# Kernel optimization log

Hardware: AMD Instinct MI355X
Metric: run time of the kernel (lower is better)

## Reference

```python
import jax, jax.numpy as jnp
import numpy as np

N_CELL, N_IO, D, H = 100000, 2000, 128, 4
C = D // H  # head dim = 32
E_CC, E_CIO, E_IOC = 600000, 50000, 50000


def _gat(x_src, x_dst, ei, W, a_src, a_dst, b, n_dst):
    """PyG GATConv (shared lin, concat=True, add_self_loops=False, eval mode)."""
    s, d = ei[0], ei[1]
    hs = (x_src @ W).reshape(-1, H, C)   # [Ns,H,C]
    hd = (x_dst @ W).reshape(-1, H, C)   # [Nd,H,C]
    al_s = (hs * a_src).sum(-1)          # [Ns,H]
    al_d = (hd * a_dst).sum(-1)          # [Nd,H]
    e = jax.nn.leaky_relu(al_s[s] + al_d[d], 0.2)            # [E,H]
    m = jax.ops.segment_max(e, d, num_segments=n_dst)
    m = jnp.where(jnp.isfinite(m), m, 0.0)
    ex = jnp.exp(e - m[d])
    den = jax.ops.segment_sum(ex, d, num_segments=n_dst)
    alpha = ex / (den[d] + 1e-16)                            # segment softmax
    out = jax.ops.segment_sum(alpha[:, :, None] * hs[s], d, num_segments=n_dst)
    return out.reshape(n_dst, D) + b


def _transform(x, Wt, bt, g, be):
    h = x @ Wt + bt
    mu = h.mean(-1, keepdims=True)
    var = h.var(-1, keepdims=True)
    h = (h - mu) * jax.lax.rsqrt(var + 1e-5) * g + be
    return x + jax.nn.relu(h)


def setup_inputs() -> dict:
    key = jax.random.key(0)
    ks = jax.random.split(key, 32)
    sc = 1.0 / np.sqrt(D)
    inp = {
        'x_cell': jax.random.normal(ks[0], (N_CELL, D), jnp.float32),
        'x_io': jax.random.normal(ks[1], (N_IO, D), jnp.float32),
        'ei_cc': jnp.stack([jax.random.randint(ks[2], (E_CC,), 0, N_CELL),
                             jax.random.randint(ks[3], (E_CC,), 0, N_CELL)]).astype(jnp.int32),
        'ei_cio': jnp.stack([jax.random.randint(ks[4], (E_CIO,), 0, N_CELL),
                              jax.random.randint(ks[5], (E_CIO,), 0, N_IO)]).astype(jnp.int32),
        'ei_ioc': jnp.stack([jax.random.randint(ks[6], (E_IOC,), 0, N_IO),
                              jax.random.randint(ks[7], (E_IOC,), 0, N_CELL)]).astype(jnp.int32),
    }
    i = 8
    for rel in ('cc', 'cio', 'ioc'):
        inp[f'W_{rel}'] = jax.random.normal(ks[i], (D, D), jnp.float32) * sc; i += 1
        inp[f'as_{rel}'] = jax.random.normal(ks[i], (H, C), jnp.float32) * sc; i += 1
        inp[f'ad_{rel}'] = jax.random.normal(ks[i], (H, C), jnp.float32) * sc; i += 1
        inp[f'b_{rel}'] = jnp.zeros((D,), jnp.float32)
    for nt in ('cell', 'io'):
        inp[f'Wt_{nt}'] = jax.random.normal(ks[i], (D, D), jnp.float32) * sc; i += 1
        inp[f'bt_{nt}'] = jnp.zeros((D,), jnp.float32)
        inp[f'g_{nt}'] = jnp.ones((D,), jnp.float32)
        inp[f'be_{nt}'] = jnp.zeros((D,), jnp.float32)
    return inp


def reference(x_cell, x_io,
              W_cc, as_cc, ad_cc, b_cc,
              W_cio, as_cio, ad_cio, b_cio,
              W_ioc, as_ioc, ad_ioc, b_ioc,
              Wt_cell, bt_cell, g_cell, be_cell,
              Wt_io, bt_io, g_io, be_io,
              ei_cc, ei_cio, ei_ioc):
    # HeteroConv with aggr='sum': cell gets cc + io->cell; io gets cell->io
    out_cell = _gat(x_cell, x_cell, ei_cc, W_cc, as_cc, ad_cc, b_cc, N_CELL) \
             + _gat(x_io, x_cell, ei_ioc, W_ioc, as_ioc, ad_ioc, b_ioc, N_CELL)
    out_io = _gat(x_cell, x_io, ei_cio, W_cio, as_cio, ad_cio, b_cio, N_IO)
    out_cell = _transform(out_cell, Wt_cell, bt_cell, g_cell, be_cell)
    out_io = _transform(out_io, Wt_io, bt_io, g_io, be_io)
    return out_cell, out_io
```

## Files before the change

### kernel.cpp

```cpp
#include <hip/hip_runtime.h>


#define NC   100000
#define NIO  2000
#define ECC  600000
#define ECIO 50000
#define EIOC 50000

#define PAD_CC   100352
#define PAD_IO   2048
#define NTOT_PAD (2 * PAD_CC + PAD_IO)
#define SCAN_NBLK (NTOT_PAD / 2048)

typedef unsigned short u16;
typedef short bf16x8 __attribute__((ext_vector_type(8)));
typedef float f32x4 __attribute__((ext_vector_type(4)));

static __device__ __forceinline__ u16 f2bf(float x) {
  unsigned u = __float_as_uint(x);
  return (u16)((u + 0x7FFFu + ((u >> 16) & 1u)) >> 16);
}
static __device__ __forceinline__ float bf2f(u16 h) {
  return __uint_as_float(((unsigned)h) << 16);
}

__global__ __launch_bounds__(256) void prep_w(
    const float* __restrict__ W0, const float* __restrict__ W1,
    const float* __restrict__ W2, const float* __restrict__ W3,
    const float* __restrict__ W4, u16* __restrict__ wt,
    const float* __restrict__ ad_ioc, const float* __restrict__ ad_cio,
    float* __restrict__ Vd_ioc, float* __restrict__ Vd_cio) {
  int t = blockIdx.x * blockDim.x + threadIdx.x;
  int mat = t >> 14, e = t & 16383;
  int k = e >> 7, n = e & 127;
  const float* W = (mat == 0) ? W0 : (mat == 1) ? W1 : (mat == 2) ? W2
                 : (mat == 3) ? W3 : W4;
  float x = W[k * 128 + n];
  u16 h = f2bf(x);
  u16 l = f2bf(x - bf2f(h));
  int kt = k >> 6, kl = k & 63, kg = kl >> 3, j = kl & 7;
  int off = (kt * 128 + n) * 64 + ((kg ^ (n & 7)) * 8) + j;
  u16* base = wt + (size_t)mat * 32768;
  base[off] = h;
  base[16384 + off] = l;

  if (t < 1024) {
    const float* Wv = (t < 512) ? W2 : W1;
    const float* ad = (t < 512) ? ad_ioc : ad_cio;
    float*       V  = (t < 512) ? Vd_ioc : Vd_cio;
    int i = t & 511, kk = i >> 2, hh = i & 3;
    float s = 0.f;
#pragma unroll
    for (int c = 0; c < 32; ++c) s += Wv[kk * 128 + hh * 32 + c] * ad[hh * 32 + c];
    V[kk * 4 + hh] = s;
  }
}

template <int MODE>
__global__ __launch_bounds__(256) void mfma_gemm(
    const float* __restrict__ A, int M,
    const u16* __restrict__ WT,
    float* __restrict__ Out,
    const float* __restrict__ as_vec, float* __restrict__ als,
    const float* __restrict__ ad_vec, float* __restrict__ ald,
    const float* __restrict__ bt, const float* __restrict__ gv_,
    const float* __restrict__ bev) {
  __shared__ u16 smem[32768];
  u16* Ah = smem;
  u16* Al = smem + 8192;
  u16* Wh = smem + 16384;
  u16* Wl = smem + 24576;
  const int tid = threadIdx.x;
  const int bm = blockIdx.x * 128;
  const int lane = tid & 63;
  const int wv = tid >> 6;
  const int qm = wv >> 1, qn = wv & 1;
  const int l15 = lane & 15, l4 = lane >> 4;

  f32x4 acc[4][4];
#pragma unroll
  for (int mi = 0; mi < 4; ++mi)
#pragma unroll
    for (int ni = 0; ni < 4; ++ni) acc[mi][ni] = {0.f, 0.f, 0.f, 0.f};

  for (int kt = 0; kt < 2; ++kt) {
#pragma unroll
    for (int q = 0; q < 4; ++q) {
      int flat = q * 256 + tid;
      int row = flat >> 3, kg = flat & 7;
      int grow = bm + row;
      float f[8];
      if (grow < M) {
        float4 v0 = *(const float4*)(A + (size_t)grow * 128 + kt * 64 + kg * 8);
        float4 v1 = *(const float4*)(A + (size_t)grow * 128 + kt * 64 + kg * 8 + 4);
        f[0] = v0.x; f[1] = v0.y; f[2] = v0.z; f[3] = v0.w;
        f[4] = v1.x; f[5] = v1.y; f[6] = v1.z; f[7] = v1.w;
      } else {
#pragma unroll
        for (int j = 0; j < 8; ++j) f[j] = 0.f;
      }
      union { bf16x8 v; u16 u[8]; } ph, pl;
#pragma unroll
      for (int j = 0; j < 8; ++j) {
        u16 h = f2bf(f[j]);
        ph.u[j] = h;
        pl.u[j] = f2bf(f[j] - bf2f(h));
      }
      int off = row * 64 + ((kg ^ (row & 7)) * 8);
      *(bf16x8*)(Ah + off) = ph.v;
      *(bf16x8*)(Al + off) = pl.v;
    }
    {
      const int4* sh = (const int4*)(WT + kt * 8192);
      const int4* sl = (const int4*)(WT + 16384 + kt * 8192);
#pragma unroll
      for (int q = 0; q < 4; ++q) {
        int idx = q * 256 + tid;
        ((int4*)Wh)[idx] = sh[idx];
        ((int4*)Wl)[idx] = sl[idx];
      }
    }
    __syncthreads();
#pragma unroll
    for (int kk = 0; kk < 2; ++kk) {
      bf16x8 ah[4], al[4], bh[4], bl[4];
#pragma unroll
      for (int mi = 0; mi < 4; ++mi) {
        int row = qm * 64 + mi * 16 + l15;
        int off = row * 64 + (((kk * 4 + l4) ^ (row & 7)) * 8);
        ah[mi] = *(const bf16x8*)(Ah + off);
        al[mi] = *(const bf16x8*)(Al + off);
      }
#pragma unroll
      for (int ni = 0; ni < 4; ++ni) {
        int n = qn * 64 + ni * 16 + l15;
        int off = n * 64 + (((kk * 4 + l4) ^ (n & 7)) * 8);
        bh[ni] = *(const bf16x8*)(Wh + off);
        bl[ni] = *(const bf16x8*)(Wl + off);
      }
#pragma unroll
      for (int mi = 0; mi < 4; ++mi)
#pragma unroll
        for (int ni = 0; ni < 4; ++ni) {
          acc[mi][ni] = __builtin_amdgcn_mfma_f32_16x16x32_bf16(
              ah[mi], bh[ni], acc[mi][ni], 0, 0, 0);
          acc[mi][ni] = __builtin_amdgcn_mfma_f32_16x16x32_bf16(
              ah[mi], bl[ni], acc[mi][ni], 0, 0, 0);
          acc[mi][ni] = __builtin_amdgcn_mfma_f32_16x16x32_bf16(
              al[mi], bh[ni], acc[mi][ni], 0, 0, 0);
        }
    }
    __syncthreads();
  }

  if (MODE == 1) {
#pragma unroll
    for (int mi = 0; mi < 4; ++mi)
#pragma unroll
      for (int ni = 0; ni < 4; ++ni)
#pragma unroll
        for (int r = 0; r < 4; ++r) {
          int grow = bm + qm * 64 + mi * 16 + l4 * 4 + r;
          if (grow < M)
            Out[(size_t)grow * 128 + qn * 64 + ni * 16 + l15] = acc[mi][ni][r];
        }
    float asv[4], adv[4];
#pragma unroll
    for (int ni = 0; ni < 4; ++ni) {
      asv[ni] = as_vec[qn * 64 + ni * 16 + l15];
      adv[ni] = (ald != nullptr) ? ad_vec[qn * 64 + ni * 16 + l15] : 0.f;
    }
#pragma unroll
    for (int mi = 0; mi < 4; ++mi)
#pragma unroll
      for (int r = 0; r < 4; ++r) {
        float s0 = acc[mi][0][r] * asv[0] + acc[mi][1][r] * asv[1];
        float s1 = acc[mi][2][r] * asv[2] + acc[mi][3][r] * asv[3];
        float t0 = acc[mi][0][r] * adv[0] + acc[mi][1][r] * adv[1];
        float t1 = acc[mi][2][r] * adv[2] + acc[mi][3][r] * adv[3];
#pragma unroll
        for (int off = 1; off < 16; off <<= 1) {
          s0 += __shfl_xor(s0, off);
          s1 += __shfl_xor(s1, off);
          t0 += __shfl_xor(t0, off);
          t1 += __shfl_xor(t1, off);
        }
        if (l15 == 0) {
          int grow = bm + qm * 64 + mi * 16 + l4 * 4 + r;
          if (grow < M) {
            als[(size_t)grow * 4 + qn * 2]     = s0;
            als[(size_t)grow * 4 + qn * 2 + 1] = s1;
            if (ald != nullptr) {
              ald[(size_t)grow * 4 + qn * 2]     = t0;
              ald[(size_t)grow * 4 + qn * 2 + 1] = t1;
            }
          }
        }
      }
  } else {
    float btv[4], gvv[4], bevv[4];
#pragma unroll
    for (int ni = 0; ni < 4; ++ni) {
      int col = qn * 64 + ni * 16 + l15;
      btv[ni] = bt[col]; gvv[ni] = gv_[col]; bevv[ni] = bev[col];
    }
    float* part = (float*)(smem + 16384);
#pragma unroll
    for (int mi = 0; mi < 4; ++mi)
#pragma unroll
      for (int r = 0; r < 4; ++r) {
        float hs = 0.f, hss = 0.f;
#pragma unroll
        for (int ni = 0; ni < 4; ++ni) {
          float hv = acc[mi][ni][r] + btv[ni];
          hs += hv; hss += hv * hv;
        }
#pragma unroll
        for (int off = 1; off < 16; off <<= 1) {
          hs += __shfl_xor(hs, off);
          hss += __shfl_xor(hss, off);
        }
        if (l15 == 0) {
          int rl = qm * 64 + mi * 16 + l4 * 4 + r;
          part[rl * 4 + qn * 2]     = hs;
          part[rl * 4 + qn * 2 + 1] = hss;
        }
      }
    __syncthreads();
#pragma unroll
    for (int mi = 0; mi < 4; ++mi)
#pragma unroll
      for (int r = 0; r < 4; ++r) {
        int rl = qm * 64 + mi * 16 + l4 * 4 + r;
        int grow = bm + rl;
        float s  = part[rl * 4] + part[rl * 4 + 2];
        float ss = part[rl * 4 + 1] + part[rl * 4 + 3];
        float mu = s * (1.f / 128.f);
        float var = ss * (1.f / 128.f) - mu * mu;
        float rs = rsqrtf(var + 1e-5f);
        if (grow < M) {
#pragma unroll
          for (int ni = 0; ni < 4; ++ni) {
            int col = qn * 64 + ni * 16 + l15;
            float y = A[(size_t)grow * 128 + col];
            float hv = acc[mi][ni][r] + btv[ni];
            float hn = (hv - mu) * rs * gvv[ni] + bevv[ni];
            Out[(size_t)grow * 128 + col] = y + (hn > 0.f ? hn : 0.f);
          }
        }
      }
  }
}

__global__ __launch_bounds__(256) void gemv_all(
    const float* __restrict__ x_cell, const float* __restrict__ x_io,
    const float* __restrict__ Vd_ioc, const float* __restrict__ Vd_cio,
    float* __restrict__ ald_ioc, float* __restrict__ ald_cio) {
  int lane = threadIdx.x & 63;
  int wid  = (blockIdx.x * blockDim.x + threadIdx.x) >> 6;
  int nw   = (gridDim.x * blockDim.x) >> 6;
  for (int row = wid; row < NC + NIO; row += nw) {
    const float* xr; const float* Vd; float* o;
    if (row < NC) { xr = x_cell + (size_t)row * 128; Vd = Vd_ioc; o = ald_ioc + 4 * (size_t)row; }
    else { int r2 = row - NC; xr = x_io + (size_t)r2 * 128; Vd = Vd_cio; o = ald_cio + 4 * (size_t)r2; }
    float4 v0 = *(const float4*)(Vd + 8 * lane);
    float4 v1 = *(const float4*)(Vd + 8 * lane + 4);
    float2 xv = *(const float2*)(xr + 2 * lane);
    float p0 = xv.x * v0.x + xv.y * v1.x;
    float p1 = xv.x * v0.y + xv.y * v1.y;
    float p2 = xv.x * v0.z + xv.y * v1.z;
    float p3 = xv.x * v0.w + xv.y * v1.w;
#pragma unroll
    for (int off = 32; off >= 1; off >>= 1) {
      p0 += __shfl_xor(p0, off);
      p1 += __shfl_xor(p1, off);
      p2 += __shfl_xor(p2, off);
      p3 += __shfl_xor(p3, off);
    }
    if (lane == 0) *(float4*)o = make_float4(p0, p1, p2, p3);
  }
}

__global__ void hist_all(const int* __restrict__ ei_cc, const int* __restrict__ ei_ioc,
                         const int* __restrict__ ei_cio,
                         int* __restrict__ c_cc, int* __restrict__ c_ioc,
                         int* __restrict__ c_cio) {
  int i = blockIdx.x * blockDim.x + threadIdx.x;
  if (i < ECC) atomicAdd(c_cc + ei_cc[ECC + i], 1);
  else if (i < ECC + EIOC) { int j = i - ECC; atomicAdd(c_ioc + ei_ioc[EIOC + j], 1); }
  else if (i < ECC + EIOC + ECIO) { int j = i - ECC - EIOC; atomicAdd(c_cio + ei_cio[ECIO + j], 1); }
}

__global__ __launch_bounds__(1024) void scan_p1(const int* __restrict__ cnt,
                                                int* __restrict__ bsum) {
  int b = blockIdx.x, t = threadIdx.x;
  int2 c = *(const int2*)(cnt + (size_t)b * 2048 + 2 * t);
  int v = c.x + c.y;
#pragma unroll
  for (int off = 1; off < 64; off <<= 1) v += __shfl_xor(v, off);
  __shared__ int ws_[16];
  if ((t & 63) == 0) ws_[t >> 6] = v;
  __syncthreads();
  if (t < 16) {
    int x = ws_[t];
#pragma unroll
    for (int off = 1; off < 16; off <<= 1) x += __shfl_xor(x, off);
    if (t == 0) bsum[b] = x;
  }
}

__global__ __launch_bounds__(1024) void scan_p3(
    const int* __restrict__ cnt, const int* __restrict__ bsum,
    int* __restrict__ roff_cc, int* __restrict__ wp_cc,
    int* __restrict__ roff_ioc, int* __restrict__ wp_ioc,
    int* __restrict__ roff_cio, int* __restrict__ wp_cio) {
  int b = blockIdx.x, t = threadIdx.x;
  __shared__ int topbase_s;
  if (t < 64) {
    int s = 0;
    if (t < b) s += bsum[t];
    if (t + 64 < b) s += bsum[t + 64];
#pragma unroll
    for (int off = 1; off < 64; off <<= 1) s += __shfl_xor(s, off);
    if (t == 0) topbase_s = s;
  }
  int gbase = b * 2048;
  int2 c = *(const int2*)(cnt + (size_t)gbase + 2 * t);
  int s = c.x + c.y;
  int lane = t & 63, wv = t >> 6;
  int inc = s;
#pragma unroll
  for (int off = 1; off < 64; off <<= 1) {
    int u = __shfl_up(inc, off);
    if (lane >= off) inc += u;
  }
  __shared__ int wsum[16];
  if (lane == 63) wsum[wv] = inc;
  __syncthreads();
  if (t == 0) {
    int run = 0;
#pragma unroll
    for (int i = 0; i < 16; ++i) { int x = wsum[i]; wsum[i] = run; run += x; }
  }
  __syncthreads();
  int excl = inc - s + wsum[wv] + topbase_s;

  int *roff, *wp;
  int rstart, rn, bsub;
  if (b < PAD_CC / 2048) {
    roff = roff_cc;  wp = wp_cc;  rstart = 0;          rn = NC;  bsub = 0;
  } else if (b < 2 * (PAD_CC / 2048)) {
    roff = roff_ioc; wp = wp_ioc; rstart = PAD_CC;     rn = NC;  bsub = ECC;
  } else {
    roff = roff_cio; wp = wp_cio; rstart = 2 * PAD_CC; rn = NIO; bsub = ECC + EIOC;
  }
  int li0 = gbase + 2 * t - rstart;
  int e0 = excl - bsub, e1 = excl + c.x - bsub;
  if (li0 < rn)     { roff[li0]     = e0; wp[li0]     = e0; }
  if (li0 + 1 < rn) { roff[li0 + 1] = e1; wp[li0 + 1] = e1; }
  if (b == 0 && t == 0) {
    roff_cc[NC]   = ECC;
    roff_ioc[NC]  = EIOC;
    roff_cio[NIO] = ECIO;
  }
}

__global__ void scatter_all(const int* __restrict__ ei_cc, const int* __restrict__ ei_ioc,
                            const int* __restrict__ ei_cio,
                            int* __restrict__ wp_cc, int* __restrict__ wp_ioc,
                            int* __restrict__ wp_cio,
                            int* __restrict__ s_cc, int* __restrict__ s_ioc,
                            int* __restrict__ s_cio) {
  int i = blockIdx.x * blockDim.x + threadIdx.x;
  if (i < ECC) {
// ... 26 lines not shown
    for (int j = 0; j < cn; ++j) {
      int s = __shfl(my_s, j);
      float v = als[4 * (size_t)s + h] + aldh;
      v = v > 0.f ? v : 0.2f * v;
      float ex = __expf(v);
      den += ex;
      float2 hv = *(const float2*)(Hs + (size_t)s * 128 + 2 * lane);
      acc0 += ex * hv.x;
      acc1 += ex * hv.y;
    }
  }
  float inv = 1.f / (den + 1e-16f);
  return make_float2(acc0 * inv, acc1 * inv);
}

__global__ __launch_bounds__(256) void dest_agg_cell(
    const int* __restrict__ roff1, const int* __restrict__ ssrc1,
    const float* __restrict__ als1, const float* __restrict__ ald1,
    const float* __restrict__ H1, const float* __restrict__ b1,
    const int* __restrict__ roff2, const int* __restrict__ ssrc2,
    const float* __restrict__ als2, const float* __restrict__ ald2,
    const float* __restrict__ H2, const float* __restrict__ b2,
    float* __restrict__ Y, int M) {
  int lane = threadIdx.x & 63;
  int wid  = (blockIdx.x * blockDim.x + threadIdx.x) >> 6;
  int nw   = (gridDim.x * blockDim.x) >> 6;
  int h    = lane >> 4;
  float2 bb1 = *(const float2*)(b1 + 2 * lane);
  float2 bb2 = *(const float2*)(b2 + 2 * lane);
  for (int d = wid; d < M; d += nw) {
    float2 c1 = gat_contrib(d, lane, h, roff1, ssrc1, als1, ald1, H1);
    float2 c2 = gat_contrib(d, lane, h, roff2, ssrc2, als2, ald2, H2);
    *(float2*)(Y + (size_t)d * 128 + 2 * lane) =
        make_float2(c1.x + c2.x + bb1.x + bb2.x, c1.y + c2.y + bb1.y + bb2.y);
  }
}

__global__ __launch_bounds__(256) void dest_agg_io(
    const int* __restrict__ roff, const int* __restrict__ ssrc,
    const float* __restrict__ als, const float* __restrict__ ald,
    const float* __restrict__ H, const float* __restrict__ b,
    float* __restrict__ Y, int M) {
  int lane = threadIdx.x & 63;
  int wid  = (blockIdx.x * blockDim.x + threadIdx.x) >> 6;
  int nw   = (gridDim.x * blockDim.x) >> 6;
  int h    = lane >> 4;
  float2 bb = *(const float2*)(b + 2 * lane);
  for (int d = wid; d < M; d += nw) {
    float2 c = gat_contrib(d, lane, h, roff, ssrc, als, ald, H);
    *(float2*)(Y + (size_t)d * 128 + 2 * lane) = make_float2(c.x + bb.x, c.y + bb.y);
  }
}

extern "C" void kernel_launch(void* const* d_in, const int* in_sizes, int n_in,
                              void* d_out, int out_size, void* d_ws, size_t ws_size,
                              hipStream_t stream) {
  const float* x_cell = (const float*)d_in[0];
  const float* x_io   = (const float*)d_in[1];
  const int*   ei_cc  = (const int*)d_in[2];
  const int*   ei_cio = (const int*)d_in[3];
  const int*   ei_ioc = (const int*)d_in[4];
  const float* W_cc   = (const float*)d_in[5];
  const float* as_cc  = (const float*)d_in[6];
  const float* ad_cc  = (const float*)d_in[7];
  const float* b_cc   = (const float*)d_in[8];
// ... 44 lines not shown
  int* wp_cc    = ib + io_; io_ += NC;
  int* roff_ioc = ib + io_; io_ += NC + 1;
  int* wp_ioc   = ib + io_; io_ += NC;
  int* roff_cio = ib + io_; io_ += NIO + 1;
  int* wp_cio   = ib + io_; io_ += NIO;
  int* ssrc_cc  = ib + io_; io_ += ECC;
  int* ssrc_ioc = ib + io_; io_ += EIOC;
  int* ssrc_cio = ib + io_; io_ += ECIO;

  u16* WT_cc  = wt_base;
  u16* WT_cio = wt_base + 32768;
  u16* WT_ioc = wt_base + 2 * 32768;
  u16* WT_tc  = wt_base + 3 * 32768;
  u16* WT_ti  = wt_base + 4 * 32768;

  hipMemsetAsync(cnt_all, 0, (size_t)NTOT_PAD * sizeof(int), stream);
  prep_w<<<320, 256, 0, stream>>>(W_cc, W_cio, W_ioc, Wt_cell, Wt_io, wt_base,
                                  ad_ioc, ad_cio, Vd_ioc, Vd_cio);

  hist_all<<<(ECC + EIOC + ECIO + 255) / 256, 256, 0, stream>>>(
      ei_cc, ei_ioc, ei_cio, cnt_cc, cnt_ioc, cnt_cio);
  scan_p1<<<SCAN_NBLK, 1024, 0, stream>>>(cnt_all, bsum);
  scan_p3<<<SCAN_NBLK, 1024, 0, stream>>>(cnt_all, bsum, roff_cc, wp_cc,
                                          roff_ioc, wp_ioc, roff_cio, wp_cio);
  scatter_all<<<(ECC + EIOC + ECIO + 255) / 256, 256, 0, stream>>>(
      ei_cc, ei_ioc, ei_cio, wp_cc, wp_ioc, wp_cio, ssrc_cc, ssrc_ioc, ssrc_cio);

  mfma_gemm<1><<<(NC + 127) / 128, 256, 0, stream>>>(
      x_cell, NC, WT_cc, Hcc, as_cc, als_cc, ad_cc, ald_cc,
      nullptr, nullptr, nullptr);
  mfma_gemm<1><<<(NC + 127) / 128, 256, 0, stream>>>(
      x_cell, NC, WT_cio, Hcio, as_cio, als_cio, nullptr, nullptr,
      nullptr, nullptr, nullptr);
  mfma_gemm<1><<<(NIO + 127) / 128, 256, 0, stream>>>(
      x_io, NIO, WT_ioc, Hioc, as_ioc, als_ioc, nullptr, nullptr,
      nullptr, nullptr, nullptr);
  gemv_all<<<2048, 256, 0, stream>>>(x_cell, x_io, Vd_ioc, Vd_cio,
                                     ald_ioc, ald_cio);

  dest_agg_cell<<<(NC + 3) / 4, 256, 0, stream>>>(
      roff_cc, ssrc_cc, als_cc, ald_cc, Hcc, b_cc,
      roff_ioc, ssrc_ioc, als_ioc, ald_ioc, Hioc, b_ioc, Ycell, NC);
  dest_agg_io<<<(NIO + 3) / 4, 256, 0, stream>>>(
      roff_cio, ssrc_cio, als_cio, ald_cio, Hcio, b_cio, Yio, NIO);

  mfma_gemm<2><<<(NC + 127) / 128, 256, 0, stream>>>(
      Ycell, NC, WT_tc, out_cell, nullptr, nullptr, nullptr, nullptr,
      bt_cell, g_cell, be_cell);
  mfma_gemm<2><<<(NIO + 127) / 128, 256, 0, stream>>>(
      Yio, NIO, WT_ti, out_io, nullptr, nullptr, nullptr, nullptr,
      bt_io, g_io, be_io);
}
```

Baseline: 472.1 us.

## Merge launches into union kernels and share x_cell staging across two GEMMs

Cuts the launch count by merging independent stages into block-range-dispatched kernels. The memset joins weight prep, and histogram, projection GEMMs and gemv share one launch. The two aggregations form one kernel, as do the two transform GEMMs. The cc and cio projections of x_cell now run in one dual GEMM that stages A once and reuses it for both weight matrices. The scan kernels use 256 threads each handling 8 counts. The dual GEMM doubles accumulator registers and may cut occupancy, and the heterogeneous union kernels may carry register pressure across branches.

New measurement: 481.8 us. +2.1%, slower.

```diff
diff --git a/kernel.cpp b/kernel.cpp
--- a/kernel.cpp
+++ b/kernel.cpp
@@ -12,6 +12,17 @@
 #define NTOT_PAD (2 * PAD_CC + PAD_IO)
 #define SCAN_NBLK (NTOT_PAD / 2048)
 
+#define GB_PREP 320
+#define GB_ZERO 198
+#define GB_DUAL 782
+#define GB_IOC  16
+#define GB_GEMV 1024
+#define GB_HIST 2735
+#define GB_AGGC 25000
+#define GB_AGGI 500
+#define GB_TC   782
+#define GB_TI   16
+
 typedef unsigned short u16;
 typedef short bf16x8 __attribute__((ext_vector_type(8)));
 typedef float f32x4 __attribute__((ext_vector_type(4)));
@@ -24,298 +35,373 @@
   return __uint_as_float(((unsigned)h) << 16);
 }
 
-__global__ __launch_bounds__(256) void prep_w(
+static __device__ __forceinline__ void stage_A(const float* __restrict__ A, int M,
+                                               int bm, int kt, int tid,
+                                               u16* Ah, u16* Al) {
+#pragma unroll
+  for (int q = 0; q < 4; ++q) {
+    int flat = q * 256 + tid;
+    int row = flat >> 3, kg = flat & 7;
+    int grow = bm + row;
+    float f[8];
+    if (grow < M) {
+      float4 v0 = *(const float4*)(A + (size_t)grow * 128 + kt * 64 + kg * 8);
+      float4 v1 = *(const float4*)(A + (size_t)grow * 128 + kt * 64 + kg * 8 + 4);
+      f[0] = v0.x; f[1] = v0.y; f[2] = v0.z; f[3] = v0.w;
+      f[4] = v1.x; f[5] = v1.y; f[6] = v1.z; f[7] = v1.w;
+    } else {
+#pragma unroll
+      for (int j = 0; j < 8; ++j) f[j] = 0.f;
+    }
+    union { bf16x8 v; u16 u[8]; } ph, pl;
+#pragma unroll
+    for (int j = 0; j < 8; ++j) {
+      u16 h = f2bf(f[j]);
+      ph.u[j] = h;
+      pl.u[j] = f2bf(f[j] - bf2f(h));
+    }
+    int off = row * 64 + ((kg ^ (row & 7)) * 8);
+    *(bf16x8*)(Ah + off) = ph.v;
+    *(bf16x8*)(Al + off) = pl.v;
+  }
+}
+
+static __device__ __forceinline__ void stage_W(const u16* __restrict__ WT, int kt,
+                                               int tid, u16* Wh, u16* Wl) {
+  const int4* sh = (const int4*)(WT + kt * 8192);
+  const int4* sl = (const int4*)(WT + 16384 + kt * 8192);
+#pragma unroll
+  for (int q = 0; q < 4; ++q) {
+    int idx = q * 256 + tid;
+    ((int4*)Wh)[idx] = sh[idx];
+    ((int4*)Wl)[idx] = sl[idx];
+  }
+}
+
+static __device__ __forceinline__ void mfma_tile(const u16* Ah, const u16* Al,
+                                                 const u16* Wh, const u16* Wl,
+                                                 int qm, int qn, int l15, int l4,
+                                                 f32x4 (&acc)[4][4]) {
+#pragma unroll
+  for (int kk = 0; kk < 2; ++kk) {
+    bf16x8 ah[4], al[4], bh[4], bl[4];
+#pragma unroll
+    for (int mi = 0; mi < 4; ++mi) {
+      int row = qm * 64 + mi * 16 + l15;
+      int off = row * 64 + (((kk * 4 + l4) ^ (row & 7)) * 8);
+      ah[mi] = *(const bf16x8*)(Ah + off);
+      al[mi] = *(const bf16x8*)(Al + off);
+    }
+#pragma unroll
+    for (int ni = 0; ni < 4; ++ni) {
+      int n = qn * 64 + ni * 16 + l15;
+      int off = n * 64 + (((kk * 4 + l4) ^ (n & 7)) * 8);
+      bh[ni] = *(const bf16x8*)(Wh + off);
+      bl[ni] = *(const bf16x8*)(Wl + off);
+    }
+#pragma unroll
+    for (int mi = 0; mi < 4; ++mi)
+#pragma unroll
+      for (int ni = 0; ni < 4; ++ni) {
+        acc[mi][ni] = __builtin_amdgcn_mfma_f32_16x16x32_bf16(
+            ah[mi], bh[ni], acc[mi][ni], 0, 0, 0);
+        acc[mi][ni] = __builtin_amdgcn_mfma_f32_16x16x32_bf16(
+            ah[mi], bl[ni], acc[mi][ni], 0, 0, 0);
+        acc[mi][ni] = __builtin_amdgcn_mfma_f32_16x16x32_bf16(
+            al[mi], bh[ni], acc[mi][ni], 0, 0, 0);
+      }
+  }
+}
+
+static __device__ void epilogue1(f32x4 (&acc)[4][4], int bm, int M,
+                                 float* __restrict__ Out,
+                                 const float* __restrict__ as_vec, float* __restrict__ als,
+                                 const float* __restrict__ ad_vec, float* __restrict__ ald) {
+  const int tid = threadIdx.x, lane = tid & 63, wv = tid >> 6;
+  const int qm = wv >> 1, qn = wv & 1, l15 = lane & 15, l4 = lane >> 4;
+#pragma unroll
+  for (int mi = 0; mi < 4; ++mi)
+#pragma unroll
+    for (int ni = 0; ni < 4; ++ni)
+#pragma unroll
+      for (int r = 0; r < 4; ++r) {
+        int grow = bm + qm * 64 + mi * 16 + l4 * 4 + r;
+        if (grow < M)
+          Out[(size_t)grow * 128 + qn * 64 + ni * 16 + l15] = acc[mi][ni][r];
+      }
+  float asv[4], adv[4];
+#pragma unroll
+  for (int ni = 0; ni < 4; ++ni) {
+    asv[ni] = as_vec[qn * 64 + ni * 16 + l15];
+    adv[ni] = (ald != nullptr) ? ad_vec[qn * 64 + ni * 16 + l15] : 0.f;
+  }
+#pragma unroll
+  for (int mi = 0; mi < 4; ++mi)
+#pragma unroll
+    for (int r = 0; r < 4; ++r) {
+      float s0 = acc[mi][0][r] * asv[0] + acc[mi][1][r] * asv[1];
+      float s1 = acc[mi][2][r] * asv[2] + acc[mi][3][r] * asv[3];
+      float t0 = acc[mi][0][r] * adv[0] + acc[mi][1][r] * adv[1];
+      float t1 = acc[mi][2][r] * adv[2] + acc[mi][3][r] * adv[3];
+#pragma unroll
+      for (int off = 1; off < 16; off <<= 1) {
+        s0 += __shfl_xor(s0, off);
+        s1 += __shfl_xor(s1, off);
+        t0 += __shfl_xor(t0, off);
+        t1 += __shfl_xor(t1, off);
+      }
+      if (l15 == 0) {
+        int grow = bm + qm * 64 + mi * 16 + l4 * 4 + r;
+        if (grow < M) {
+          als[(size_t)grow * 4 + qn * 2]     = s0;
+          als[(size_t)grow * 4 + qn * 2 + 1] = s1;
+          if (ald != nullptr) {
+            ald[(size_t)grow * 4 + qn * 2]     = t0;
+            ald[(size_t)grow * 4 + qn * 2 + 1] = t1;
+          }
+        }
+      }
+    }
+}
+
+static __device__ void epilogue2(f32x4 (&acc)[4][4], int bm, int M,
+                                 const float* __restrict__ A, float* __restrict__ Out,
+                                 const float* __restrict__ bt, const float* __restrict__ gv_,
+                                 const float* __restrict__ bev, u16* smem) {
+  const int tid = threadIdx.x, lane = tid & 63, wv = tid >> 6;
+  const int qm = wv >> 1, qn = wv & 1, l15 = lane & 15, l4 = lane >> 4;
+  float btv[4], gvv[4], bevv[4];
+#pragma unroll
+  for (int ni = 0; ni < 4; ++ni) {
+    int col = qn * 64 + ni * 16 + l15;
+    btv[ni] = bt[col]; gvv[ni] = gv_[col]; bevv[ni] = bev[col];
+  }
+  float* part = (float*)(smem + 16384);
+#pragma unroll
+  for (int mi = 0; mi < 4; ++mi)
+#pragma unroll
+    for (int r = 0; r < 4; ++r) {
+      float hs = 0.f, hss = 0.f;
+#pragma unroll
+      for (int ni = 0; ni < 4; ++ni) {
+        float hv = acc[mi][ni][r] + btv[ni];
+        hs += hv; hss += hv * hv;
+      }
+#pragma unroll
+      for (int off = 1; off < 16; off <<= 1) {
+        hs += __shfl_xor(hs, off);
+        hss += __shfl_xor(hss, off);
+      }
+      if (l15 == 0) {
+        int rl = qm * 64 + mi * 16 + l4 * 4 + r;
+        part[rl * 4 + qn * 2]     = hs;
+        part[rl * 4 + qn * 2 + 1] = hss;
+      }
+    }
+  __syncthreads();
+#pragma unroll
+  for (int mi = 0; mi < 4; ++mi)
+#pragma unroll
+    for (int r = 0; r < 4; ++r) {
+      int rl = qm * 64 + mi * 16 + l4 * 4 + r;
+      int grow = bm + rl;
+      float s  = part[rl * 4] + part[rl * 4 + 2];
+      float ss = part[rl * 4 + 1] + part[rl * 4 + 3];
+      float mu = s * (1.f / 128.f);
+      float var = ss * (1.f / 128.f) - mu * mu;
+      float rs = rsqrtf(var + 1e-5f);
+      if (grow < M) {
+#pragma unroll
+        for (int ni = 0; ni < 4; ++ni) {
+          int col = qn * 64 + ni * 16 + l15;
+          float y = A[(size_t)grow * 128 + col];
+          float hv = acc[mi][ni][r] + btv[ni];
+          float hn = (hv - mu) * rs * gvv[ni] + bevv[ni];
+          Out[(size_t)grow * 128 + col] = y + (hn > 0.f ? hn : 0.f);
+        }
+      }
+    }
+}
+
+template <int MODE>
+static __device__ void gemm_body(int bx, const float* __restrict__ A, int M,
+                                 const u16* __restrict__ WT, float* __restrict__ Out,
+                                 const float* as_vec, float* als,
+                                 const float* ad_vec, float* ald,
+                                 const float* bt, const float* gv_, const float* bev,
+                                 u16* smem) {
+  u16* Ah = smem;
+  u16* Al = smem + 8192;
+  u16* Wh = smem + 16384;
+  u16* Wl = smem + 24576;
+  const int tid = threadIdx.x, bm = bx * 128, lane = tid & 63, wv = tid >> 6;
+  const int qm = wv >> 1, qn = wv & 1, l15 = lane & 15, l4 = lane >> 4;
+  f32x4 acc[4][4];
+#pragma unroll
+  for (int mi = 0; mi < 4; ++mi)
+#pragma unroll
+    for (int ni = 0; ni < 4; ++ni) acc[mi][ni] = {0.f, 0.f, 0.f, 0.f};
+  for (int kt = 0; kt < 2; ++kt) {
+    stage_A(A, M, bm, kt, tid, Ah, Al);
+    stage_W(WT, kt, tid, Wh, Wl);
+    __syncthreads();
+    mfma_tile(Ah, Al, Wh, Wl, qm, qn, l15, l4, acc);
+    __syncthreads();
+  }
+  if (MODE == 1) epilogue1(acc, bm, M, Out, as_vec, als, ad_vec, ald);
+  else           epilogue2(acc, bm, M, A, Out, bt, gv_, bev, smem);
+}
+
+static __device__ void gemm_dual_body(int bx, const float* __restrict__ A, int M,
+                                      const u16* __restrict__ WT0, const u16* __restrict__ WT1,
+                                      float* __restrict__ H0, float* __restrict__ H1,
+                                      const float* as0, float* als0,
+                                      const float* ad0, float* ald0,
+                                      const float* as1, float* als1, u16* smem) {
+  u16* Ah = smem;
+  u16* Al = smem + 8192;
+  u16* Wh = smem + 16384;
+  u16* Wl = smem + 24576;
+  const int tid = threadIdx.x, bm = bx * 128, lane = tid & 63, wv = tid >> 6;
+  const int qm = wv >> 1, qn = wv & 1, l15 = lane & 15, l4 = lane >> 4;
+  f32x4 acc0[4][4], acc1[4][4];
+#pragma unroll
+  for (int mi = 0; mi < 4; ++mi)
+#pragma unroll
+    for (int ni = 0; ni < 4; ++ni) {
+      acc0[mi][ni] = {0.f, 0.f, 0.f, 0.f};
+      acc1[mi][ni] = {0.f, 0.f, 0.f, 0.f};
+    }
+  for (int kt = 0; kt < 2; ++kt) {
+    stage_A(A, M, bm, kt, tid, Ah, Al);
+    stage_W(WT0, kt, tid, Wh, Wl);
+    __syncthreads();
+    mfma_tile(Ah, Al, Wh, Wl, qm, qn, l15, l4, acc0);
+    __syncthreads();
+    stage_W(WT1, kt, tid, Wh, Wl);
+    __syncthreads();
+    mfma_tile(Ah, Al, Wh, Wl, qm, qn, l15, l4, acc1);
+    __syncthreads();
+  }
+  epilogue1(acc0, bm, M, H0, as0, als0, ad0, ald0);
+  epilogue1(acc1, bm, M, H1, as1, als1, nullptr, nullptr);
+}
+
+__global__ __launch_bounds__(256) void k1_prep(
     const float* __restrict__ W0, const float* __restrict__ W1,
     const float* __restrict__ W2, const float* __restrict__ W3,
     const float* __restrict__ W4, u16* __restrict__ wt,
     const float* __restrict__ ad_ioc, const float* __restrict__ ad_cio,
-    float* __restrict__ Vd_ioc, float* __restrict__ Vd_cio) {
-  int t = blockIdx.x * blockDim.x + threadIdx.x;
-  int mat = t >> 14, e = t & 16383;
-  int k = e >> 7, n = e & 127;
-  const float* W = (mat == 0) ? W0 : (mat == 1) ? W1 : (mat == 2) ? W2
-                 : (mat == 3) ? W3 : W4;
-  float x = W[k * 128 + n];
-  u16 h = f2bf(x);
-  u16 l = f2bf(x - bf2f(h));
-  int kt = k >> 6, kl = k & 63, kg = kl >> 3, j = kl & 7;
-  int off = (kt * 128 + n) * 64 + ((kg ^ (n & 7)) * 8) + j;
-  u16* base = wt + (size_t)mat * 32768;
-  base[off] = h;
-  base[16384 + off] = l;
-
-  if (t < 1024) {
-    const float* Wv = (t < 512) ? W2 : W1;
-    const float* ad = (t < 512) ? ad_ioc : ad_cio;
-    float*       V  = (t < 512) ? Vd_ioc : Vd_cio;
-    int i = t & 511, kk = i >> 2, hh = i & 3;
-    float s = 0.f;
-#pragma unroll
-    for (int c = 0; c < 32; ++c) s += Wv[kk * 128 + hh * 32 + c] * ad[hh * 32 + c];
-    V[kk * 4 + hh] = s;
-  }
-}
-
-template <int MODE>
-__global__ __launch_bounds__(256) void mfma_gemm(
-    const float* __restrict__ A, int M,
-    const u16* __restrict__ WT,
-    float* __restrict__ Out,
-    const float* __restrict__ as_vec, float* __restrict__ als,
-    const float* __restrict__ ad_vec, float* __restrict__ ald,
-    const float* __restrict__ bt, const float* __restrict__ gv_,
-    const float* __restrict__ bev) {
+    float* __restrict__ Vd_ioc, float* __restrict__ Vd_cio,
+    int* __restrict__ cnt_all) {
+  int b = blockIdx.x;
+  if (b < GB_PREP) {
+    int t = b * 256 + threadIdx.x;
+    int mat = t >> 14, e = t & 16383;
+    int k = e >> 7, n = e & 127;
+    const float* W = (mat == 0) ? W0 : (mat == 1) ? W1 : (mat == 2) ? W2
+                   : (mat == 3) ? W3 : W4;
+    float x = W[k * 128 + n];
+    u16 h = f2bf(x);
+    u16 l = f2bf(x - bf2f(h));
+    int kt = k >> 6, kl = k & 63, kg = kl >> 3, j = kl & 7;
+    int off = (kt * 128 + n) * 64 + ((kg ^ (n & 7)) * 8) + j;
+    u16* base = wt + (size_t)mat * 32768;
+    base[off] = h;
+    base[16384 + off] = l;
+    if (t < 1024) {
+      const float* Wv = (t < 512) ? W2 : W1;
+      const float* ad = (t < 512) ? ad_ioc : ad_cio;
+      float*       V  = (t < 512) ? Vd_ioc : Vd_cio;
+      int i = t & 511, kk = i >> 2, hh = i & 3;
+      float s = 0.f;
+#pragma unroll
+      for (int c = 0; c < 32; ++c) s += Wv[kk * 128 + hh * 32 + c] * ad[hh * 32 + c];
+      V[kk * 4 + hh] = s;
+    }
+  } else {
+    int i = (b - GB_PREP) * 256 + threadIdx.x;
+    ((int4*)cnt_all)[i] = make_int4(0, 0, 0, 0);
+  }
+}
+
+__global__ __launch_bounds__(256) void k2_union(
+    const float* __restrict__ x_cell, const float* __restrict__ x_io,
+    const u16* __restrict__ WT_cc, const u16* __restrict__ WT_cio,
+    const u16* __restrict__ WT_ioc,
+    float* __restrict__ Hcc, float* __restrict__ Hcio, float* __restrict__ Hioc,
+    const float* __restrict__ as_cc, float* __restrict__ als_cc,
+    const float* __restrict__ ad_cc, float* __restrict__ ald_cc,
+    const float* __restrict__ as_cio, float* __restrict__ als_cio,
+    const float* __restrict__ as_ioc, float* __restrict__ als_ioc,
+    const float* __restrict__ Vd_ioc, const float* __restrict__ Vd_cio,
+    float* __restrict__ ald_ioc, float* __restrict__ ald_cio,
+    const int* __restrict__ ei_cc, const int* __restrict__ ei_ioc,
+    const int* __restrict__ ei_cio,
+    int* __restrict__ c_cc, int* __restrict__ c_ioc, int* __restrict__ c_cio) {
   __shared__ u16 smem[32768];
-  u16* Ah = smem;
-  u16* Al = smem + 8192;
-  u16* Wh = smem + 16384;
-  u16* Wl = smem + 24576;
-  const int tid = threadIdx.x;
-  const int bm = blockIdx.x * 128;
-  const int lane = tid & 63;
-  const int wv = tid >> 6;
-  const int qm = wv >> 1, qn = wv & 1;
-  const int l15 = lane & 15, l4 = lane >> 4;
-
-  f32x4 acc[4][4];
-#pragma unroll
-  for (int mi = 0; mi < 4; ++mi)
-#pragma unroll
-    for (int ni = 0; ni < 4; ++ni) acc[mi][ni] = {0.f, 0.f, 0.f, 0.f};
-
-  for (int kt = 0; kt < 2; ++kt) {
-#pragma unroll
-    for (int q = 0; q < 4; ++q) {
-      int flat = q * 256 + tid;
-      int row = flat >> 3, kg = flat & 7;
-      int grow = bm + row;
-      float f[8];
-      if (grow < M) {
-        float4 v0 = *(const float4*)(A + (size_t)grow * 128 + kt * 64 + kg * 8);
-        float4 v1 = *(const float4*)(A + (size_t)grow * 128 + kt * 64 + kg * 8 + 4);
-        f[0] = v0.x; f[1] = v0.y; f[2] = v0.z; f[3] = v0.w;
-        f[4] = v1.x; f[5] = v1.y; f[6] = v1.z; f[7] = v1.w;
-      } else {
-#pragma unroll
-        for (int j = 0; j < 8; ++j) f[j] = 0.f;
-      }
-      union { bf16x8 v; u16 u[8]; } ph, pl;
-#pragma unroll
-      for (int j = 0; j < 8; ++j) {
-        u16 h = f2bf(f[j]);
-        ph.u[j] = h;
-        pl.u[j] = f2bf(f[j] - bf2f(h));
-      }
-      int off = row * 64 + ((kg ^ (row & 7)) * 8);
-      *(bf16x8*)(Ah + off) = ph.v;
-      *(bf16x8*)(Al + off) = pl.v;
-    }
-    {
-      const int4* sh = (const int4*)(WT + kt * 8192);
-      const int4* sl = (const int4*)(WT + 16384 + kt * 8192);
-#pragma unroll
-      for (int q = 0; q < 4; ++q) {
-        int idx = q * 256 + tid;
-        ((int4*)Wh)[idx] = sh[idx];
-        ((int4*)Wl)[idx] = sl[idx];
-      }
-    }
-    __syncthreads();
-#pragma unroll
-    for (int kk = 0; kk < 2; ++kk) {
-      bf16x8 ah[4], al[4], bh[4], bl[4];
-#pragma unroll
-      for (int mi = 0; mi < 4; ++mi) {
-        int row = qm * 64 + mi * 16 + l15;
-        int off = row * 64 + (((kk * 4 + l4) ^ (row & 7)) * 8);
-        ah[mi] = *(const bf16x8*)(Ah + off);
-        al[mi] = *(const bf16x8*)(Al + off);
-      }
-#pragma unroll
-      for (int ni = 0; ni < 4; ++ni) {
-        int n = qn * 64 + ni * 16 + l15;
-        int off = n * 64 + (((kk * 4 + l4) ^ (n & 7)) * 8);
-        bh[ni] = *(const bf16x8*)(Wh + off);
-        bl[ni] = *(const bf16x8*)(Wl + off);
-      }
-#pragma unroll
-      for (int mi = 0; mi < 4; ++mi)
-#pragma unroll
-        for (int ni = 0; ni < 4; ++ni) {
-          acc[mi][ni] = __builtin_amdgcn_mfma_f32_16x16x32_bf16(
-              ah[mi], bh[ni], acc[mi][ni], 0, 0, 0);
-          acc[mi][ni] = __builtin_amdgcn_mfma_f32_16x16x32_bf16(
-              ah[mi], bl[ni], acc[mi][ni], 0, 0, 0);
-          acc[mi][ni] = __builtin_amdgcn_mfma_f32_16x16x32_bf16(
-              al[mi], bh[ni], acc[mi][ni], 0, 0, 0);
-        }
-    }
-    __syncthreads();
-  }
-
-  if (MODE == 1) {
-#pragma unroll
-    for (int mi = 0; mi < 4; ++mi)
-#pragma unroll
-      for (int ni = 0; ni < 4; ++ni)
-#pragma unroll
-        for (int r = 0; r < 4; ++r) {
-          int grow = bm + qm * 64 + mi * 16 + l4 * 4 + r;
-          if (grow < M)
-            Out[(size_t)grow * 128 + qn * 64 + ni * 16 + l15] = acc[mi][ni][r];
-        }
-    float asv[4], adv[4];
-#pragma unroll
-    for (int ni = 0; ni < 4; ++ni) {
-      asv[ni] = as_vec[qn * 64 + ni * 16 + l15];
-      adv[ni] = (ald != nullptr) ? ad_vec[qn * 64 + ni * 16 + l15] : 0.f;
-    }
-#pragma unroll
-    for (int mi = 0; mi < 4; ++mi)
-#pragma unroll
-      for (int r = 0; r < 4; ++r) {
-        float s0 = acc[mi][0][r] * asv[0] + acc[mi][1][r] * asv[1];
-        float s1 = acc[mi][2][r] * asv[2] + acc[mi][3][r] * asv[3];
-        float t0 = acc[mi][0][r] * adv[0] + acc[mi][1][r] * adv[1];
-        float t1 = acc[mi][2][r] * adv[2] + acc[mi][3][r] * adv[3];
-#pragma unroll
-        for (int off = 1; off < 16; off <<= 1) {
-          s0 += __shfl_xor(s0, off);
-          s1 += __shfl_xor(s1, off);
-          t0 += __shfl_xor(t0, off);
-          t1 += __shfl_xor(t1, off);
-        }
-        if (l15 == 0) {
-          int grow = bm + qm * 64 + mi * 16 + l4 * 4 + r;
-          if (grow < M) {
-            als[(size_t)grow * 4 + qn * 2]     = s0;
-            als[(size_t)grow * 4 + qn * 2 + 1] = s1;
-            if (ald != nullptr) {
-              ald[(size_t)grow * 4 + qn * 2]     = t0;
-              ald[(size_t)grow * 4 + qn * 2 + 1] = t1;
-            }
-          }
-        }
-      }
+  int b = blockIdx.x;
+  if (b < GB_DUAL) {
+    gemm_dual_body(b, x_cell, NC, WT_cc, WT_cio, Hcc, Hcio,
+                   as_cc, als_cc, ad_cc, ald_cc, as_cio, als_cio, smem);
+  } else if (b < GB_DUAL + GB_IOC) {
+    gemm_body<1>(b - GB_DUAL, x_io, NIO, WT_ioc, Hioc, as_ioc, als_ioc,
+                 nullptr, nullptr, nullptr, nullptr, nullptr, smem);
+  } else if (b < GB_DUAL + GB_IOC + GB_GEMV) {
+    int lb = b - GB_DUAL - GB_IOC;
+    int lane = threadIdx.x & 63;
+    int wid  = (lb * 256 + (int)threadIdx.x) >> 6;
+    int nw   = GB_GEMV * 4;
+    for (int row = wid; row < NC + NIO; row += nw) {
+      const float* xr; const float* Vd; float* o;
+      if (row < NC) { xr = x_cell + (size_t)row * 128; Vd = Vd_ioc; o = ald_ioc + 4 * (size_t)row; }
+      else { int r2 = row - NC; xr = x_io + (size_t)r2 * 128; Vd = Vd_cio; o = ald_cio + 4 * (size_t)r2; }
+      float4 v0 = *(const float4*)(Vd + 8 * lane);
+      float4 v1 = *(const float4*)(Vd + 8 * lane + 4);
+      float2 xv = *(const float2*)(xr + 2 * lane);
+      float p0 = xv.x * v0.x + xv.y * v1.x;
+      float p1 = xv.x * v0.y + xv.y * v1.y;
+      float p2 = xv.x * v0.z + xv.y * v1.z;
+      float p3 = xv.x * v0.w + xv.y * v1.w;
+#pragma unroll
+      for (int off = 32; off >= 1; off >>= 1) {
+        p0 += __shfl_xor(p0, off);
+        p1 += __shfl_xor(p1, off);
+        p2 += __shfl_xor(p2, off);
+        p3 += __shfl_xor(p3, off);
+      }
+      if (lane == 0) *(float4*)o = make_float4(p0, p1, p2, p3);
+    }
   } else {
-    float btv[4], gvv[4], bevv[4];
-#pragma unroll
-    for (int ni = 0; ni < 4; ++ni) {
-      int col = qn * 64 + ni * 16 + l15;
-      btv[ni] = bt[col]; gvv[ni] = gv_[col]; bevv[ni] = bev[col];
-    }
-    float* part = (float*)(smem + 16384);
-#pragma unroll
-    for (int mi = 0; mi < 4; ++mi)
-#pragma unroll
-      for (int r = 0; r < 4; ++r) {
-        float hs = 0.f, hss = 0.f;
-#pragma unroll
-        for (int ni = 0; ni < 4; ++ni) {
-          float hv = acc[mi][ni][r] + btv[ni];
-          hs += hv; hss += hv * hv;
-        }
-#pragma unroll
-        for (int off = 1; off < 16; off <<= 1) {
-          hs += __shfl_xor(hs, off);
-          hss += __shfl_xor(hss, off);
-        }
-        if (l15 == 0) {
-          int rl = qm * 64 + mi * 16 + l4 * 4 + r;
-          part[rl * 4 + qn * 2]     = hs;
-          part[rl * 4 + qn * 2 + 1] = hss;
-        }
-      }
-    __syncthreads();
-#pragma unroll
-    for (int mi = 0; mi < 4; ++mi)
-#pragma unroll
-      for (int r = 0; r < 4; ++r) {
-        int rl = qm * 64 + mi * 16 + l4 * 4 + r;
-        int grow = bm + rl;
-        float s  = part[rl * 4] + part[rl * 4 + 2];
-        float ss = part[rl * 4 + 1] + part[rl * 4 + 3];
-        float mu = s * (1.f / 128.f);
-        float var = ss * (1.f / 128.f) - mu * mu;
-        float rs = rsqrtf(var + 1e-5f);
-        if (grow < M) {
-#pragma unroll
-          for (int ni = 0; ni < 4; ++ni) {
-            int col = qn * 64 + ni * 16 + l15;
-            float y = A[(size_t)grow * 128 + col];
-            float hv = acc[mi][ni][r] + btv[ni];
-            float hn = (hv - mu) * rs * gvv[ni] + bevv[ni];
-            Out[(size_t)grow * 128 + col] = y + (hn > 0.f ? hn : 0.f);
-          }
-        }
-      }
-  }
-}
-
-__global__ __launch_bounds__(256) void gemv_all(
-    const float* __restrict__ x_cell, const float* __restrict__ x_io,
-    const float* __restrict__ Vd_ioc, const float* __restrict__ Vd_cio,
-    float* __restrict__ ald_ioc, float* __restrict__ ald_cio) {
-  int lane = threadIdx.x & 63;
-  int wid  = (blockIdx.x * blockDim.x + threadIdx.x) >> 6;
-  int nw   = (gridDim.x * blockDim.x) >> 6;
-  for (int row = wid; row < NC + NIO; row += nw) {
-    const float* xr; const float* Vd; float* o;
-    if (row < NC) { xr = x_cell + (size_t)row * 128; Vd = Vd_ioc; o = ald_ioc + 4 * (size_t)row; }
-    else { int r2 = row - NC; xr = x_io + (size_t)r2 * 128; Vd = Vd_cio; o = ald_cio + 4 * (size_t)r2; }
-    float4 v0 = *(const float4*)(Vd + 8 * lane);
-    float4 v1 = *(const float4*)(Vd + 8 * lane + 4);
-    float2 xv = *(const float2*)(xr + 2 * lane);
-    float p0 = xv.x * v0.x + xv.y * v1.x;
-    float p1 = xv.x * v0.y + xv.y * v1.y;
-    float p2 = xv.x * v0.z + xv.y * v1.z;
-    float p3 = xv.x * v0.w + xv.y * v1.w;
-#pragma unroll
-    for (int off = 32; off >= 1; off >>= 1) {
-      p0 += __shfl_xor(p0, off);
-      p1 += __shfl_xor(p1, off);
-      p2 += __shfl_xor(p2, off);
-      p3 += __shfl_xor(p3, off);
-    }
-    if (lane == 0) *(float4*)o = make_float4(p0, p1, p2, p3);
-  }
-}
-
-__global__ void hist_all(const int* __restrict__ ei_cc, const int* __restrict__ ei_ioc,
-                         const int* __restrict__ ei_cio,
-                         int* __restrict__ c_cc, int* __restrict__ c_ioc,
-                         int* __restrict__ c_cio) {
-  int i = blockIdx.x * blockDim.x + threadIdx.x;
-  if (i < ECC) atomicAdd(c_cc + ei_cc[ECC + i], 1);
-  else if (i < ECC + EIOC) { int j = i - ECC; atomicAdd(c_ioc + ei_ioc[EIOC + j], 1); }
-  else if (i < ECC + EIOC + ECIO) { int j = i - ECC - EIOC; atomicAdd(c_cio + ei_cio[ECIO + j], 1); }
-}
-
-__global__ __launch_bounds__(1024) void scan_p1(const int* __restrict__ cnt,
-                                                int* __restrict__ bsum) {
+    int i = (b - GB_DUAL - GB_IOC - GB_GEMV) * 256 + threadIdx.x;
+    if (i < ECC) atomicAdd(c_cc + ei_cc[ECC + i], 1);
+    else if (i < ECC + EIOC) { int j = i - ECC; atomicAdd(c_ioc + ei_ioc[EIOC + j], 1); }
+    else if (i < ECC + EIOC + ECIO) { int j = i - ECC - EIOC; atomicAdd(c_cio + ei_cio[ECIO + j], 1); }
+  }
+}
+
+__global__ __launch_bounds__(256) void scan_p1(const int* __restrict__ cnt,
+                                               int* __restrict__ bsum) {
   int b = blockIdx.x, t = threadIdx.x;
-  int2 c = *(const int2*)(cnt + (size_t)b * 2048 + 2 * t);
-  int v = c.x + c.y;
-#pragma unroll
-  for (int off = 1; off < 64; off <<= 1) v += __shfl_xor(v, off);
-  __shared__ int ws_[16];
-  if ((t & 63) == 0) ws_[t >> 6] = v;
+  const int4* p = (const int4*)(cnt + (size_t)b * 2048) + t * 2;
+  int4 a = p[0], c = p[1];
+  int s = a.x + a.y + a.z + a.w + c.x + c.y + c.z + c.w;
+#pragma unroll
+  for (int off = 1; off < 64; off <<= 1) s += __shfl_xor(s, off);
+  __shared__ int ws_[4];
+  if ((t & 63) == 0) ws_[t >> 6] = s;
   __syncthreads();
-  if (t < 16) {
-    int x = ws_[t];
-#pragma unroll
-    for (int off = 1; off < 16; off <<= 1) x += __shfl_xor(x, off);
-    if (t == 0) bsum[b] = x;
-  }
-}
-
-__global__ __launch_bounds__(1024) void scan_p3(
+  if (t == 0) bsum[b] = ws_[0] + ws_[1] + ws_[2] + ws_[3];
+}
+
+__global__ __launch_bounds__(256) void scan_p3(
     const int* __restrict__ cnt, const int* __restrict__ bsum,
     int* __restrict__ roff_cc, int* __restrict__ wp_cc,
     int* __restrict__ roff_ioc, int* __restrict__ wp_ioc,
     int* __restrict__ roff_cio, int* __restrict__ wp_cio) {
   int b = blockIdx.x, t = threadIdx.x;
   __shared__ int topbase_s;
+  __shared__ int wsum[4];
   if (t < 64) {
     int s = 0;
     if (t < b) s += bsum[t];
@@ -325,8 +411,10 @@
     if (t == 0) topbase_s = s;
   }
   int gbase = b * 2048;
-  int2 c = *(const int2*)(cnt + (size_t)gbase + 2 * t);
-  int s = c.x + c.y;
+  const int4* p = (const int4*)(cnt + (size_t)gbase) + t * 2;
+  int4 a = p[0], c = p[1];
+  int cs[8] = {a.x, a.y, a.z, a.w, c.x, c.y, c.z, c.w};
+  int s = cs[0] + cs[1] + cs[2] + cs[3] + cs[4] + cs[5] + cs[6] + cs[7];
   int lane = t & 63, wv = t >> 6;
   int inc = s;
 #pragma unroll
@@ -334,13 +422,12 @@
     int u = __shfl_up(inc, off);
     if (lane >= off) inc += u;
   }
-  __shared__ int wsum[16];
   if (lane == 63) wsum[wv] = inc;
   __syncthreads();
   if (t == 0) {
     int run = 0;
 #pragma unroll
-    for (int i = 0; i < 16; ++i) { int x = wsum[i]; wsum[i] = run; run += x; }
+    for (int i = 0; i < 4; ++i) { int x = wsum[i]; wsum[i] = run; run += x; }
   }
   __syncthreads();
   int excl = inc - s + wsum[wv] + topbase_s;
@@ -354,10 +441,13 @@
   } else {
     roff = roff_cio; wp = wp_cio; rstart = 2 * PAD_CC; rn = NIO; bsub = ECC + EIOC;
   }
-  int li0 = gbase + 2 * t - rstart;
-  int e0 = excl - bsub, e1 = excl + c.x - bsub;
-  if (li0 < rn)     { roff[li0]     = e0; wp[li0]     = e0; }
-  if (li0 + 1 < rn) { roff[li0 + 1] = e1; wp[li0 + 1] = e1; }
+  int li0 = gbase + t * 8 - rstart;
+  int run = excl - bsub;
+#pragma unroll
+  for (int j = 0; j < 8; ++j) {
+    if (li0 + j < rn) { roff[li0 + j] = run; wp[li0 + j] = run; }
+    run += cs[j];
+  }
   if (b == 0 && t == 0) {
     roff_cc[NC]   = ECC;
     roff_ioc[NC]  = EIOC;
@@ -414,41 +504,56 @@
   return make_float2(acc0 * inv, acc1 * inv);
 }
 
-__global__ __launch_bounds__(256) void dest_agg_cell(
+__global__ __launch_bounds__(256) void k_agg(
     const int* __restrict__ roff1, const int* __restrict__ ssrc1,
     const float* __restrict__ als1, const float* __restrict__ ald1,
     const float* __restrict__ H1, const float* __restrict__ b1,
     const int* __restrict__ roff2, const int* __restrict__ ssrc2,
     const float* __restrict__ als2, const float* __restrict__ ald2,
     const float* __restrict__ H2, const float* __restrict__ b2,
-    float* __restrict__ Y, int M) {
+    float* __restrict__ Ycell,
+    const int* __restrict__ roff3, const int* __restrict__ ssrc3,
+    const float* __restrict__ als3, const float* __restrict__ ald3,
+    const float* __restrict__ H3, const float* __restrict__ b3,
+    float* __restrict__ Yio) {
+  int b = blockIdx.x;
   int lane = threadIdx.x & 63;
-  int wid  = (blockIdx.x * blockDim.x + threadIdx.x) >> 6;
-  int nw   = (gridDim.x * blockDim.x) >> 6;
   int h    = lane >> 4;
-  float2 bb1 = *(const float2*)(b1 + 2 * lane);
-  float2 bb2 = *(const float2*)(b2 + 2 * lane);
-  for (int d = wid; d < M; d += nw) {
-    float2 c1 = gat_contrib(d, lane, h, roff1, ssrc1, als1, ald1, H1);
-    float2 c2 = gat_contrib(d, lane, h, roff2, ssrc2, als2, ald2, H2);
-    *(float2*)(Y + (size_t)d * 128 + 2 * lane) =
-        make_float2(c1.x + c2.x + bb1.x + bb2.x, c1.y + c2.y + bb1.y + bb2.y);
-  }
-}
-
-__global__ __launch_bounds__(256) void dest_agg_io(
-    const int* __restrict__ roff, const int* __restrict__ ssrc,
-    const float* __restrict__ als, const float* __restrict__ ald,
-    const float* __restrict__ H, const float* __restrict__ b,
-    float* __restrict__ Y, int M) {
-  int lane = threadIdx.x & 63;
-  int wid  = (blockIdx.x * blockDim.x + threadIdx.x) >> 6;
-  int nw   = (gridDim.x * blockDim.x) >> 6;
-  int h    = lane >> 4;
-  float2 bb = *(const float2*)(b + 2 * lane);
-  for (int d = wid; d < M; d += nw) {
-    float2 c = gat_contrib(d, lane, h, roff, ssrc, als, ald, H);
-    *(float2*)(Y + (size_t)d * 128 + 2 * lane) = make_float2(c.x + bb.x, c.y + bb.y);
+  if (b < GB_AGGC) {
+    int wid = (b * 256 + (int)threadIdx.x) >> 6;
+    float2 bb1 = *(const float2*)(b1 + 2 * lane);
+    float2 bb2 = *(const float2*)(b2 + 2 * lane);
+    for (int d = wid; d < NC; d += GB_AGGC * 4) {
+      float2 c1 = gat_contrib(d, lane, h, roff1, ssrc1, als1, ald1, H1);
+      float2 c2 = gat_contrib(d, lane, h, roff2, ssrc2, als2, ald2, H2);
+      *(float2*)(Ycell + (size_t)d * 128 + 2 * lane) =
+          make_float2(c1.x + c2.x + bb1.x + bb2.x, c1.y + c2.y + bb1.y + bb2.y);
+    }
+  } else {
+    int wid = ((b - GB_AGGC) * 256 + (int)threadIdx.x) >> 6;
+    float2 bb = *(const float2*)(b3 + 2 * lane);
+    for (int d = wid; d < NIO; d += GB_AGGI * 4) {
+      float2 c = gat_contrib(d, lane, h, roff3, ssrc3, als3, ald3, H3);
+      *(float2*)(Yio + (size_t)d * 128 + 2 * lane) = make_float2(c.x + bb.x, c.y + bb.y);
+    }
+  }
+}
+
+__global__ __launch_bounds__(256) void k_transform(
+    const float* __restrict__ Ycell, const u16* __restrict__ WT_tc,
+    const float* __restrict__ bt_c, const float* __restrict__ g_c,
+    const float* __restrict__ be_c, float* __restrict__ out_cell,
+    const float* __restrict__ Yio, const u16* __restrict__ WT_ti,
+    const float* __restrict__ bt_i, const float* __restrict__ g_i,
+    const float* __restrict__ be_i, float* __restrict__ out_io) {
+  __shared__ u16 smem[32768];
+  int b = blockIdx.x;
+  if (b < GB_TC) {
+    gemm_body<2>(b, Ycell, NC, WT_tc, out_cell, nullptr, nullptr, nullptr,
+                 nullptr, bt_c, g_c, be_c, smem);
+  } else {
+    gemm_body<2>(b - GB_TC, Yio, NIO, WT_ti, out_io, nullptr, nullptr, nullptr,
+                 nullptr, bt_i, g_i, be_i, smem);
   }
 }
 
@@ -523,40 +628,29 @@
   u16* WT_tc  = wt_base + 3 * 32768;
   u16* WT_ti  = wt_base + 4 * 32768;
 
-  hipMemsetAsync(cnt_all, 0, (size_t)NTOT_PAD * sizeof(int), stream);
-  prep_w<<<320, 256, 0, stream>>>(W_cc, W_cio, W_ioc, Wt_cell, Wt_io, wt_base,
-                                  ad_ioc, ad_cio, Vd_ioc, Vd_cio);
-
-  hist_all<<<(ECC + EIOC + ECIO + 255) / 256, 256, 0, stream>>>(
+  k1_prep<<<GB_PREP + GB_ZERO, 256, 0, stream>>>(
+      W_cc, W_cio, W_ioc, Wt_cell, Wt_io, wt_base,
+      ad_ioc, ad_cio, Vd_ioc, Vd_cio, cnt_all);
+
+  k2_union<<<GB_DUAL + GB_IOC + GB_GEMV + GB_HIST, 256, 0, stream>>>(
+      x_cell, x_io, WT_cc, WT_cio, WT_ioc, Hcc, Hcio, Hioc,
+      as_cc, als_cc, ad_cc, ald_cc, as_cio, als_cio, as_ioc, als_ioc,
+      Vd_ioc, Vd_cio, ald_ioc, ald_cio,
       ei_cc, ei_ioc, ei_cio, cnt_cc, cnt_ioc, cnt_cio);
-  scan_p1<<<SCAN_NBLK, 1024, 0, stream>>>(cnt_all, bsum);
-  scan_p3<<<SCAN_NBLK, 1024, 0, stream>>>(cnt_all, bsum, roff_cc, wp_cc,
-                                          roff_ioc, wp_ioc, roff_cio, wp_cio);
-  scatter_all<<<(ECC + EIOC + ECIO + 255) / 256, 256, 0, stream>>>(
+
+  scan_p1<<<SCAN_NBLK, 256, 0, stream>>>(cnt_all, bsum);
+  scan_p3<<<SCAN_NBLK, 256, 0, stream>>>(cnt_all, bsum, roff_cc, wp_cc,
+                                         roff_ioc, wp_ioc, roff_cio, wp_cio);
+
+  scatter_all<<<GB_HIST, 256, 0, stream>>>(
       ei_cc, ei_ioc, ei_cio, wp_cc, wp_ioc, wp_cio, ssrc_cc, ssrc_ioc, ssrc_cio);
 
-  mfma_gemm<1><<<(NC + 127) / 128, 256, 0, stream>>>(
-      x_cell, NC, WT_cc, Hcc, as_cc, als_cc, ad_cc, ald_cc,
-      nullptr, nullptr, nullptr);
-  mfma_gemm<1><<<(NC + 127) / 128, 256, 0, stream>>>(
-      x_cell, NC, WT_cio, Hcio, as_cio, als_cio, nullptr, nullptr,
-      nullptr, nullptr, nullptr);
-  mfma_gemm<1><<<(NIO + 127) / 128, 256, 0, stream>>>(
-      x_io, NIO, WT_ioc, Hioc, as_ioc, als_ioc, nullptr, nullptr,
-      nullptr, nullptr, nullptr);
-  gemv_all<<<2048, 256, 0, stream>>>(x_cell, x_io, Vd_ioc, Vd_cio,
-                                     ald_ioc, ald_cio);
-
-  dest_agg_cell<<<(NC + 3) / 4, 256, 0, stream>>>(
+  k_agg<<<GB_AGGC + GB_AGGI, 256, 0, stream>>>(
       roff_cc, ssrc_cc, als_cc, ald_cc, Hcc, b_cc,
-      roff_ioc, ssrc_ioc, als_ioc, ald_ioc, Hioc, b_ioc, Ycell, NC);
-  dest_agg_io<<<(NIO + 3) / 4, 256, 0, stream>>>(
-      roff_cio, ssrc_cio, als_cio, ald_cio, Hcio, b_cio, Yio, NIO);
-
-  mfma_gemm<2><<<(NC + 127) / 128, 256, 0, stream>>>(
-      Ycell, NC, WT_tc, out_cell, nullptr, nullptr, nullptr, nullptr,
-      bt_cell, g_cell, be_cell);
-  mfma_gemm<2><<<(NIO + 127) / 128, 256, 0, stream>>>(
-      Yio, NIO, WT_ti, out_io, nullptr, nullptr, nullptr, nullptr,
-      bt_io, g_io, be_io);
-}
+      roff_ioc, ssrc_ioc, als_ioc, ald_ioc, Hioc, b_ioc, Ycell,
+      roff_cio, ssrc_cio, als_cio, ald_cio, Hcio, b_cio, Yio);
+
+  k_transform<<<GB_TC + GB_TI, 256, 0, stream>>>(
+      Ycell, WT_tc, bt_cell, g_cell, be_cell, out_cell,
+      Yio, WT_ti, bt_io, g_io, be_io, out_io);
+}
```
